# Performance work log

Measured on AMD Instinct MI355X. Metric: run time of the kernel, lower is better.

The kernel has to match this reference:

```python
import jax, jax.numpy as jnp
import numpy as np

NH, NW = 5, 5          # attn_neighborhood_size (odd -> symmetric 'same' padding)
HEADS, HEAD_DIM = 8, 64
DIM = 512              # == heads*head_dim, but project_out=True since heads>1
B, HMAP, WMAP = 4, 64, 64
N = HMAP * WMAP


def local_expand(t, height, width):
    """Equivalent of impulse-filter conv2d neighbor gather.

    t: [b, heads, n, d] -> [b, heads, n, NH*NW, d]
    neighbor f=(i,j) of pixel (p,q) is t[p+i-NH//2, q+j-NW//2], zero-padded.
    """
    b, h, n, d = t.shape
    y = t.reshape(b, h, height, width, d)
    ph, pw = NH // 2, NW // 2
    yp = jnp.pad(y, ((0, 0), (0, 0), (ph, ph), (pw, pw), (0, 0)))
    # fixed small loop over the 25 window offsets (row-major = filter order)
    slabs = [yp[:, :, i:i + height, j:j + width, :]
             for i in range(NH) for j in range(NW)]
    out = jnp.stack(slabs, axis=4)  # [b, h, H, W, F, d]
    return out.reshape(b, h, n, NH * NW, d)


def setup_inputs() -> dict:
    key = jax.random.key(0)
    k1, k2, k3, k4 = jax.random.split(key, 4)
    inner = HEADS * HEAD_DIM
    x = jax.random.normal(k1, (B, N, DIM), dtype=jnp.float32)
    # torch Linear weights are [out_features, in_features]
    w_qkv = jax.random.normal(k2, (3 * inner, DIM), dtype=jnp.float32) * (DIM ** -0.5)
    w_out = jax.random.normal(k3, (DIM, inner), dtype=jnp.float32) * (inner ** -0.5)
    b_out = jax.random.normal(k4, (DIM,), dtype=jnp.float32) * 0.01
    return {"x": x, "w_qkv": w_qkv, "w_out": w_out, "b_out": b_out,
            "h": HMAP, "w": WMAP}


def reference(x, w_qkv, w_out, b_out, h, w):
    b, n, _ = x.shape
    scale = HEAD_DIM ** -0.5
    qkv = x @ w_qkv.T                                   # [b, n, 3*inner]
    q, k, v = jnp.split(qkv, 3, axis=-1)
    def to_heads(t):
        return t.reshape(b, n, HEADS, HEAD_DIM).transpose(0, 2, 1, 3)  # b h n d
    q, k, v = to_heads(q), to_heads(k), to_heads(v)
    k_loc = local_expand(k, h, w)                       # [b, h, n, F, d]
    v_loc = local_expand(v, h, w)
    dots = jnp.einsum('bhnd,bhnfd->bhnf', q, k_loc) * scale
    attn = jax.nn.softmax(dots, axis=-1)
    out = jnp.einsum('bhnf,bhnfd->bhnd', attn, v_loc)   # [b, h, n, d]
    out = out.transpose(0, 2, 1, 3).reshape(b, n, HEADS * HEAD_DIM)
    return out @ w_out.T + b_out                        # dropout=0 (eval)
```

## Files before the change

kernel.cpp:

```cpp
#include <hip/hip_runtime.h>
#include <cstddef>
#include <cstdint>


namespace {

typedef short s16x8 __attribute__((ext_vector_type(8)));
typedef unsigned short u16x8 __attribute__((ext_vector_type(8)));
typedef float f32x4 __attribute__((ext_vector_type(4)));

constexpr int kHeads = 8;
constexpr int kN = 4096;
constexpr float kScale = 0.125f;

__device__ inline float b2f(unsigned short u) {
  return __uint_as_float((unsigned)u << 16);
}
__device__ inline unsigned short f2b(float x) {
  unsigned u = __float_as_uint(x);
  return (unsigned short)((u + 0x7fffu + ((u >> 16) & 1u)) >> 16);
}

__device__ __forceinline__ void g2l16(const unsigned short* g,
                                      unsigned short* l) {
  __builtin_amdgcn_global_load_lds(
      (const __attribute__((address_space(1))) void*)g,
      (__attribute__((address_space(3))) void*)l, 16, 0, 0);
}

__global__ __launch_bounds__(256) void cvt_w(
    const float* __restrict__ w1, const float* __restrict__ w2,
    unsigned short* __restrict__ o1, unsigned short* __restrict__ o2) {
  const int gid = blockIdx.x * 256 + threadIdx.x;
  const int gs = gridDim.x * 256;
  for (int i = gid; i < 786432 / 4; i += gs) {
    float4 v = ((const float4*)w1)[i];
    ushort4 o;
    o.x = f2b(v.x); o.y = f2b(v.y); o.z = f2b(v.z); o.w = f2b(v.w);
    ((ushort4*)o1)[i] = o;
  }
  for (int i = gid; i < 262144 / 4; i += gs) {
    float4 v = ((const float4*)w2)[i];
    ushort4 o;
    o.x = f2b(v.x); o.y = f2b(v.y); o.z = f2b(v.z); o.w = f2b(v.w);
    ((ushort4*)o2)[i] = o;
  }
}

__global__ __launch_bounds__(256) void cvt_x(const float* __restrict__ x,
                                             unsigned short* __restrict__ xb) {
  const int i = blockIdx.x * 256 + threadIdx.x;
  const float4 a = ((const float4*)x)[i * 2];
  const float4 b = ((const float4*)x)[i * 2 + 1];
  u16x8 o;
  o[0] = f2b(a.x); o[1] = f2b(a.y); o[2] = f2b(a.z); o[3] = f2b(a.w);
  o[4] = f2b(b.x); o[5] = f2b(b.y); o[6] = f2b(b.z); o[7] = f2b(b.w);
  *(u16x8*)(xb + (size_t)i * 8) = o;
}

__device__ __forceinline__ void mfma_512(const unsigned short* __restrict__ A,
                                         const unsigned short* __restrict__ W,
                                         int m0, int n0, int tid,
                                         unsigned short* As, unsigned short* Bs,
                                         f32x4 (&acc)[4][4]) {
  const int lane = tid & 63;
  const int wv = tid >> 6;
  const int wm = wv & 1, wn = wv >> 1;
  const int rr = lane >> 2;
  const int cc = (lane & 3) * 8;
#pragma unroll
  for (int i = 0; i < 4; ++i)
#pragma unroll
    for (int j = 0; j < 4; ++j) acc[i][j] = f32x4{0.f, 0.f, 0.f, 0.f};

  for (int k0 = 0; k0 < 512; k0 += 32) {
#pragma unroll
    for (int it = 0; it < 2; ++it) {
      const int grp = wv * 2 + it;
      const int row = grp * 16 + rr;
      g2l16(A + (size_t)(m0 + row) * 512 + k0 + cc, As + grp * 512);
      g2l16(W + (size_t)(n0 + row) * 512 + k0 + cc, Bs + grp * 512);
    }
    __syncthreads();
    s16x8 af[4], bf[4];
#pragma unroll
    for (int i = 0; i < 4; ++i) {
      af[i] = *(const s16x8*)&As[(wm * 64 + i * 16 + (lane & 15)) * 32 +
                                 (lane >> 4) * 8];
      bf[i] = *(const s16x8*)&Bs[(wn * 64 + i * 16 + (lane & 15)) * 32 +
                                 (lane >> 4) * 8];
    }
#pragma unroll
    for (int i = 0; i < 4; ++i)
#pragma unroll
      for (int j = 0; j < 4; ++j)
        acc[i][j] = __builtin_amdgcn_mfma_f32_16x16x32_bf16(af[i], bf[j],
                                                            acc[i][j], 0, 0, 0);
    __syncthreads();
  }
}

__global__ __launch_bounds__(256, 4) void gemm_qkv(
    const unsigned short* __restrict__ A, const unsigned short* __restrict__ W,
    unsigned short* __restrict__ Qb, unsigned short* __restrict__ Kb,
    unsigned short* __restrict__ Vb, int mOutBase) {
  __shared__ unsigned short As[4096], Bs[4096];
  const int tid = threadIdx.x;
  const int id = blockIdx.x;
  const int xcd = id & 7;
  const int j = id >> 3;
  const int by = xcd * 8 + j / 12;
  const int bx = j % 12;
  f32x4 acc[4][4];
  mfma_512(A, W, by * 128, bx * 128, tid, As, Bs, acc);

  const int lane = tid & 63;
  const int wv = tid >> 6;
  const int wm = wv & 1, wn = wv >> 1;
  const int cn = bx * 128 + wn * 64;
  unsigned short* dst = (cn < 512) ? Qb : (cn < 1024 ? Kb : Vb);
  const int head = (cn >> 6) & 7;
  const int colb = lane & 15;
#pragma unroll
  for (int mi = 0; mi < 4; ++mi) {
#pragma unroll
    for (int r = 0; r < 4; ++r) {
      const int m = mOutBase + by * 128 + wm * 64 + mi * 16 + (lane >> 4) * 4 + r;
      const int b = m >> 12;
      const int p = m & 4095;
      unsigned short* o =
          dst + ((size_t)(b * kHeads + head) * kN + p) * 64 + colb;
#pragma unroll
      for (int ni = 0; ni < 4; ++ni) o[ni * 16] = f2b(acc[mi][ni][r]);
    }
  }
}

__global__ __launch_bounds__(256, 4) void gemm_out(
    const unsigned short* __restrict__ A, const unsigned short* __restrict__ W,
    const float* __restrict__ bias, float* __restrict__ out) {
  __shared__ unsigned short As[4096], Bs[4096];
  const int tid = threadIdx.x;
  const int id = blockIdx.x;
  const int xcd = id & 7;
  const int j = id >> 3;
  const int by = xcd * 16 + (j >> 2);
  const int bx = j & 3;
  f32x4 acc[4][4];
  mfma_512(A, W, by * 128, bx * 128, tid, As, Bs, acc);

  const int lane = tid & 63;
  const int wv = tid >> 6;
  const int wm = wv & 1, wn = wv >> 1;
  float bvr[4];
#pragma unroll
  for (int ni = 0; ni < 4; ++ni)
    bvr[ni] = bias[bx * 128 + wn * 64 + ni * 16 + (lane & 15)];
#pragma unroll
  for (int mi = 0; mi < 4; ++mi) {
#pragma unroll
    for (int r = 0; r < 4; ++r) {
      const int m = by * 128 + wm * 64 + mi * 16 + (lane >> 4) * 4 + r;
      float* o = out + (size_t)m * 512 + bx * 128 + wn * 64 + (lane & 15);
#pragma unroll
      for (int ni = 0; ni < 4; ++ni) o[ni * 16] = acc[mi][ni][r] + bvr[ni];
    }
  }
}

__global__ __launch_bounds__(256) void attn_qk(
    const unsigned short* __restrict__ Q, const unsigned short* __restrict__ K,
    unsigned short* __restrict__ attnW) {
  __shared__ unsigned short Kh[400 * 72];
  const int tid = threadIdx.x;
  const int bh = blockIdx.y;
  const int tile = blockIdx.x;
  const int ty0 = (tile >> 2) * 16, tx0 = (tile & 3) * 16;
  const size_t base = (size_t)bh * kN;

  for (int i = tid; i < 3200; i += 256) {
    const int r = i >> 3, c = i & 7;
    const int gy = ty0 - 2 + r / 20;
    const int gx = tx0 - 2 + r % 20;
    u16x8 v = {};
    if ((unsigned)gy < 64u && (unsigned)gx < 64u)
      v = *(const u16x8*)(K + (base + gy * 64 + gx) * 64 + c * 8);
    *(u16x8*)&Kh[r * 72 + c * 8] = v;
  }
  __syncthreads();

  const int pyl = tid >> 4, pxl = tid & 15;
  const int p = (ty0 + pyl) * 64 + tx0 + pxl;

  float q[64];
  {
    const unsigned short* qp = Q + (base + p) * 64;
#pragma unroll
    for (int c = 0; c < 8; ++c) {
      const u16x8 v = *(const u16x8*)(qp + c * 8);
#pragma unroll
      for (int jj = 0; jj < 8; ++jj) q[c * 8 + jj] = b2f(v[jj]);
    }
  }

  float dots[25];
  float mx = -1e30f;
#pragma unroll
  for (int fy = 0; fy < 5; ++fy) {
#pragma unroll
    for (int fx = 0; fx < 5; ++fx) {
      const unsigned short* kr = &Kh[((pyl + fy) * 20 + pxl + fx) * 72];
      float d = 0.f;
#pragma unroll
      for (int c = 0; c < 8; ++c) {
        const u16x8 kv = *(const u16x8*)(kr + c * 8);
#pragma unroll
        for (int jj = 0; jj < 8; ++jj) d = fmaf(q[c * 8 + jj], b2f(kv[jj]), d);
      }
      d *= kScale;
      dots[fy * 5 + fx] = d;
      mx = fmaxf(mx, d);
    }
  }
  float sum = 0.f;
#pragma unroll
  for (int f = 0; f < 25; ++f) {
    dots[f] = __expf(dots[f] - mx);
    sum += dots[f];
  }
  const float inv = 1.f / sum;
  unsigned short* ap = attnW + (base + p) * 32;
#pragma unroll
  for (int f = 0; f < 25; ++f) ap[f] = f2b(dots[f] * inv);
}

__global__ __launch_bounds__(256) void attn_pv(
    const unsigned short* __restrict__ V,
    const unsigned short* __restrict__ attnW,
    unsigned short* __restrict__ AO) {
  __shared__ unsigned short Vh[400 * 72];
  const int tid = threadIdx.x;
  const int bh = blockIdx.y;
  const int tile = blockIdx.x;
  const int ty0 = (tile >> 2) * 16, tx0 = (tile & 3) * 16;
  const size_t base = (size_t)bh * kN;

  for (int i = tid; i < 3200; i += 256) {
    const int r = i >> 3, c = i & 7;
    const int gy = ty0 - 2 + r / 20;
    const int gx = tx0 - 2 + r % 20;
    u16x8 v = {};
    if ((unsigned)gy < 64u && (unsigned)gx < 64u)
      v = *(const u16x8*)(V + (base + gy * 64 + gx) * 64 + c * 8);
    *(u16x8*)&Vh[r * 72 + c * 8] = v;
  }
  __syncthreads();

  const int pyl = tid >> 4, pxl = tid & 15;
  const int p = (ty0 + pyl) * 64 + tx0 + pxl;

  float w[25];
  {
    const unsigned short* ap = attnW + (base + p) * 32;
#pragma unroll
    for (int f = 0; f < 25; ++f) w[f] = b2f(ap[f]);
  }

  float o[64];
#pragma unroll
  for (int jj = 0; jj < 64; ++jj) o[jj] = 0.f;

#pragma unroll
  for (int fy = 0; fy < 5; ++fy) {
#pragma unroll
    for (int fx = 0; fx < 5; ++fx) {
      const unsigned short* vr = &Vh[((pyl + fy) * 20 + pxl + fx) * 72];
      const float wf = w[fy * 5 + fx];
#pragma unroll
      for (int c = 0; c < 8; ++c) {
        const u16x8 vv = *(const u16x8*)(vr + c * 8);
#pragma unroll
        for (int jj = 0; jj < 8; ++jj)
          o[c * 8 + jj] = fmaf(wf, b2f(vv[jj]), o[c * 8 + jj]);
      }
    }
  }

  const int b = bh >> 3, h = bh & 7;
  unsigned short* op = AO + ((size_t)(b * kN + p)) * 512 + h * 64;
#pragma unroll
  for (int c = 0; c < 8; ++c) {
    u16x8 pk;
#pragma unroll
    for (int jj = 0; jj < 8; ++jj) pk[jj] = f2b(o[c * 8 + jj]);
    *(u16x8*)(op + c * 8) = pk;
  }
}

}

extern "C" void kernel_launch(void* const* d_in, const int* in_sizes, int n_in,
                              void* d_out, int out_size, void* d_ws,
                              size_t ws_size, hipStream_t stream) {
  (void)in_sizes; (void)n_in; (void)out_size; (void)ws_size;
  const float* x = (const float*)d_in[0];
  const float* w_qkv = (const float*)d_in[1];
  const float* w_out = (const float*)d_in[2];
  const float* b_out = (const float*)d_in[3];
  float* out = (float*)d_out;

  unsigned short* ws0 = (unsigned short*)d_ws;
  unsigned short* wqkvb = ws0;
  unsigned short* woutb = ws0 + 786432;
  unsigned short* xbh   = ws0 + 1048576;
  unsigned short* Qb    = ws0 + 5242880;
  unsigned short* Kb    = ws0 + 13631488;
  unsigned short* Vb    = ws0 + 22020096;
  unsigned short* attnW = xbh;
  unsigned short* AO    = Qb;

  cvt_w<<<512, 256, 0, stream>>>(w_qkv, w_out, wqkvb, woutb);
  cvt_x<<<2048, 256, 0, stream>>>(x, xbh);
  gemm_qkv<<<768, 256, 0, stream>>>(xbh, wqkvb, Qb, Kb, Vb, 0);
  cvt_x<<<2048, 256, 0, stream>>>(x + 4194304, xbh);
  gemm_qkv<<<768, 256, 0, stream>>>(xbh, wqkvb, Qb, Kb, Vb, 8192);
  attn_qk<<<dim3(16, 32), 256, 0, stream>>>(Qb, Kb, attnW);
  attn_pv<<<dim3(16, 32), 256, 0, stream>>>(Vb, attnW, AO);
  gemm_out<<<512, 256, 0, stream>>>(AO, woutb, b_out, out);
}
```

Before: 193.9 us.

## Fuse attention QK and PV kernels, merge conversions, single QKV GEMM

Merges the QK-softmax and PV attention kernels into one kernel that keeps the normalized weights in registers and reuses one shared-memory halo buffer for K and then V. This removes the bf16 attention-weight round trip through global memory and one kernel launch. Weight and input conversions now run in a single kernel, and the QKV projection runs as one launch over the full batch instead of two halves. The workspace grows to hold all of x, Q, K, V and AO at once, and the fused attention kernel carries both the 25 scores and the 64 accumulators in registers, which raises register pressure.

```diff
diff --git a/kernel.cpp b/kernel.cpp
--- a/kernel.cpp
+++ b/kernel.cpp
@@ -28,34 +28,27 @@
       (__attribute__((address_space(3))) void*)l, 16, 0, 0);
 }
 
-__global__ __launch_bounds__(256) void cvt_w(
-    const float* __restrict__ w1, const float* __restrict__ w2,
-    unsigned short* __restrict__ o1, unsigned short* __restrict__ o2) {
-  const int gid = blockIdx.x * 256 + threadIdx.x;
-  const int gs = gridDim.x * 256;
-  for (int i = gid; i < 786432 / 4; i += gs) {
-    float4 v = ((const float4*)w1)[i];
-    ushort4 o;
-    o.x = f2b(v.x); o.y = f2b(v.y); o.z = f2b(v.z); o.w = f2b(v.w);
-    ((ushort4*)o1)[i] = o;
-  }
-  for (int i = gid; i < 262144 / 4; i += gs) {
-    float4 v = ((const float4*)w2)[i];
-    ushort4 o;
-    o.x = f2b(v.x); o.y = f2b(v.y); o.z = f2b(v.z); o.w = f2b(v.w);
-    ((ushort4*)o2)[i] = o;
-  }
-}
-
-__global__ __launch_bounds__(256) void cvt_x(const float* __restrict__ x,
-                                             unsigned short* __restrict__ xb) {
+__global__ __launch_bounds__(256) void cvt_all(
+    const float* __restrict__ wq, const float* __restrict__ wo,
+    const float* __restrict__ x, unsigned short* __restrict__ wqb,
+    unsigned short* __restrict__ wob, unsigned short* __restrict__ xb) {
   const int i = blockIdx.x * 256 + threadIdx.x;
-  const float4 a = ((const float4*)x)[i * 2];
-  const float4 b = ((const float4*)x)[i * 2 + 1];
+  const float* src;
+  unsigned short* dst;
+  int off;
+  if (i < 98304) {
+    src = wq; dst = wqb; off = i;
+  } else if (i < 131072) {
+    src = wo; dst = wob; off = i - 98304;
+  } else {
+    src = x; dst = xb; off = i - 131072;
+  }
+  const float4 a = ((const float4*)src)[off * 2];
+  const float4 b = ((const float4*)src)[off * 2 + 1];
   u16x8 o;
   o[0] = f2b(a.x); o[1] = f2b(a.y); o[2] = f2b(a.z); o[3] = f2b(a.w);
   o[4] = f2b(b.x); o[5] = f2b(b.y); o[6] = f2b(b.z); o[7] = f2b(b.w);
-  *(u16x8*)(xb + (size_t)i * 8) = o;
+  *(u16x8*)(dst + (size_t)off * 8) = o;
 }
 
 __device__ __forceinline__ void mfma_512(const unsigned short* __restrict__ A,
@@ -103,13 +96,13 @@
 __global__ __launch_bounds__(256, 4) void gemm_qkv(
     const unsigned short* __restrict__ A, const unsigned short* __restrict__ W,
     unsigned short* __restrict__ Qb, unsigned short* __restrict__ Kb,
-    unsigned short* __restrict__ Vb, int mOutBase) {
+    unsigned short* __restrict__ Vb) {
   __shared__ unsigned short As[4096], Bs[4096];
   const int tid = threadIdx.x;
   const int id = blockIdx.x;
   const int xcd = id & 7;
   const int j = id >> 3;
-  const int by = xcd * 8 + j / 12;
+  const int by = xcd * 16 + j / 12;
   const int bx = j % 12;
   f32x4 acc[4][4];
   mfma_512(A, W, by * 128, bx * 128, tid, As, Bs, acc);
@@ -125,7 +118,7 @@
   for (int mi = 0; mi < 4; ++mi) {
 #pragma unroll
     for (int r = 0; r < 4; ++r) {
-      const int m = mOutBase + by * 128 + wm * 64 + mi * 16 + (lane >> 4) * 4 + r;
+      const int m = by * 128 + wm * 64 + mi * 16 + (lane >> 4) * 4 + r;
       const int b = m >> 12;
       const int p = m & 4095;
       unsigned short* o =
@@ -168,15 +161,17 @@
   }
 }
 
-__global__ __launch_bounds__(256) void attn_qk(
+__global__ __launch_bounds__(256) void attn_fused(
     const unsigned short* __restrict__ Q, const unsigned short* __restrict__ K,
-    unsigned short* __restrict__ attnW) {
-  __shared__ unsigned short Kh[400 * 72];
+    const unsigned short* __restrict__ V, unsigned short* __restrict__ AO) {
+  __shared__ unsigned short H[400 * 72];
   const int tid = threadIdx.x;
   const int bh = blockIdx.y;
   const int tile = blockIdx.x;
   const int ty0 = (tile >> 2) * 16, tx0 = (tile & 3) * 16;
   const size_t base = (size_t)bh * kN;
+  const int pyl = tid >> 4, pxl = tid & 15;
+  const int p = (ty0 + pyl) * 64 + tx0 + pxl;
 
   for (int i = tid; i < 3200; i += 256) {
     const int r = i >> 3, c = i & 7;
@@ -185,12 +180,8 @@
     u16x8 v = {};
     if ((unsigned)gy < 64u && (unsigned)gx < 64u)
       v = *(const u16x8*)(K + (base + gy * 64 + gx) * 64 + c * 8);
-    *(u16x8*)&Kh[r * 72 + c * 8] = v;
-  }
-  __syncthreads();
-
-  const int pyl = tid >> 4, pxl = tid & 15;
-  const int p = (ty0 + pyl) * 64 + tx0 + pxl;
+    *(u16x8*)&H[r * 72 + c * 8] = v;
+  }
 
   float q[64];
   {
@@ -202,6 +193,7 @@
       for (int jj = 0; jj < 8; ++jj) q[c * 8 + jj] = b2f(v[jj]);
     }
   }
+  __syncthreads();
 
   float dots[25];
   float mx = -1e30f;
@@ -209,7 +201,7 @@
   for (int fy = 0; fy < 5; ++fy) {
 #pragma unroll
     for (int fx = 0; fx < 5; ++fx) {
-      const unsigned short* kr = &Kh[((pyl + fy) * 20 + pxl + fx) * 72];
+      const unsigned short* kr = &H[((pyl + fy) * 20 + pxl + fx) * 72];
       float d = 0.f;
 #pragma unroll
       for (int c = 0; c < 8; ++c) {
@@ -229,22 +221,10 @@
     sum += dots[f];
   }
   const float inv = 1.f / sum;
-  unsigned short* ap = attnW + (base + p) * 32;
-#pragma unroll
-  for (int f = 0; f < 25; ++f) ap[f] = f2b(dots[f] * inv);
-}
-
-__global__ __launch_bounds__(256) void attn_pv(
-    const unsigned short* __restrict__ V,
-    const unsigned short* __restrict__ attnW,
-    unsigned short* __restrict__ AO) {
-  __shared__ unsigned short Vh[400 * 72];
-  const int tid = threadIdx.x;
-  const int bh = blockIdx.y;
-  const int tile = blockIdx.x;
-  const int ty0 = (tile >> 2) * 16, tx0 = (tile & 3) * 16;
-  const size_t base = (size_t)bh * kN;
-
+#pragma unroll
+  for (int f = 0; f < 25; ++f) dots[f] *= inv;
+
+  __syncthreads();
   for (int i = tid; i < 3200; i += 256) {
     const int r = i >> 3, c = i & 7;
     const int gy = ty0 - 2 + r / 20;
@@ -252,30 +232,19 @@
     u16x8 v = {};
     if ((unsigned)gy < 64u && (unsigned)gx < 64u)
       v = *(const u16x8*)(V + (base + gy * 64 + gx) * 64 + c * 8);
-    *(u16x8*)&Vh[r * 72 + c * 8] = v;
+    *(u16x8*)&H[r * 72 + c * 8] = v;
   }
   __syncthreads();
 
-  const int pyl = tid >> 4, pxl = tid & 15;
-  const int p = (ty0 + pyl) * 64 + tx0 + pxl;
-
-  float w[25];
-  {
-    const unsigned short* ap = attnW + (base + p) * 32;
-#pragma unroll
-    for (int f = 0; f < 25; ++f) w[f] = b2f(ap[f]);
-  }
-
   float o[64];
 #pragma unroll
   for (int jj = 0; jj < 64; ++jj) o[jj] = 0.f;
-
 #pragma unroll
   for (int fy = 0; fy < 5; ++fy) {
 #pragma unroll
     for (int fx = 0; fx < 5; ++fx) {
-      const unsigned short* vr = &Vh[((pyl + fy) * 20 + pxl + fx) * 72];
-      const float wf = w[fy * 5 + fx];
+      const unsigned short* vr = &H[((pyl + fy) * 20 + pxl + fx) * 72];
+      const float wf = dots[fy * 5 + fx];
 #pragma unroll
       for (int c = 0; c < 8; ++c) {
         const u16x8 vv = *(const u16x8*)(vr + c * 8);
@@ -312,19 +281,14 @@
   unsigned short* ws0 = (unsigned short*)d_ws;
   unsigned short* wqkvb = ws0;
   unsigned short* woutb = ws0 + 786432;
-  unsigned short* xbh   = ws0 + 1048576;
-  unsigned short* Qb    = ws0 + 5242880;
-  unsigned short* Kb    = ws0 + 13631488;
-  unsigned short* Vb    = ws0 + 22020096;
-  unsigned short* attnW = xbh;
-  unsigned short* AO    = Qb;
-
-  cvt_w<<<512, 256, 0, stream>>>(w_qkv, w_out, wqkvb, woutb);
-  cvt_x<<<2048, 256, 0, stream>>>(x, xbh);
-  gemm_qkv<<<768, 256, 0, stream>>>(xbh, wqkvb, Qb, Kb, Vb, 0);
-  cvt_x<<<2048, 256, 0, stream>>>(x + 4194304, xbh);
-  gemm_qkv<<<768, 256, 0, stream>>>(xbh, wqkvb, Qb, Kb, Vb, 8192);
-  attn_qk<<<dim3(16, 32), 256, 0, stream>>>(Qb, Kb, attnW);
-  attn_pv<<<dim3(16, 32), 256, 0, stream>>>(Vb, attnW, AO);
+  unsigned short* xb = ws0 + 1048576;
+  unsigned short* Qb = ws0 + 9437184;
+  unsigned short* Kb = ws0 + 17825792;
+  unsigned short* Vb = ws0 + 26214400;
+  unsigned short* AO = ws0 + 34603008;
+
+  cvt_all<<<4608, 256, 0, stream>>>(w_qkv, w_out, x, wqkvb, woutb, xb);
+  gemm_qkv<<<1536, 256, 0, stream>>>(xb, wqkvb, Qb, Kb, Vb);
+  attn_fused<<<dim3(16, 32), 256, 0, stream>>>(Qb, Kb, Vb, AO);
   gemm_out<<<512, 256, 0, stream>>>(AO, woutb, b_out, out);
 }
```

Result: slower. 252.0 us (+29.9%).
